# Kernel tuning notes

Hardware: AMD Instinct MI355X
Metric: run time of the kernel (lower is better)

The kernel has to match this reference:

```python
import jax, jax.numpy as jnp
import numpy as np

D_MODEL = 768
NUM_HEADS = 12
DIM_QKV = D_MODEL // NUM_HEADS  # 64
NEG_INF = -1000000000.0


def setup_inputs() -> dict:
    key = jax.random.key(0)
    ks = jax.random.split(key, 12)
    B, S = 2, 2048
    def lin(kw, kb):
        # torch nn.Linear default init: U(-1/sqrt(fan_in), 1/sqrt(fan_in))
        bound = 1.0 / np.sqrt(D_MODEL)
        W = jax.random.uniform(kw, (D_MODEL, D_MODEL), jnp.float32, -bound, bound)
        b = jax.random.uniform(kb, (D_MODEL,), jnp.float32, -bound, bound)
        return W, b
    Wq, bq = lin(ks[0], ks[1])
    Wk, bk = lin(ks[2], ks[3])
    Wv, bv = lin(ks[4], ks[5])
    Wo, bo = lin(ks[6], ks[7])
    Q = jax.random.normal(ks[8], (B, S, D_MODEL), jnp.float32)
    K = jax.random.normal(ks[9], (B, S, D_MODEL), jnp.float32)
    V = jax.random.normal(ks[10], (B, S, D_MODEL), jnp.float32)
    mask = jnp.tril(jnp.ones((S, S), dtype=bool))[None, None]  # [1,1,S,S] causal
    return {"Q": Q, "K": K, "V": V, "mask": mask,
            "Wq": Wq, "bq": bq, "Wk": Wk, "bk": bk,
            "Wv": Wv, "bv": bv, "Wo": Wo, "bo": bo}


def _split_heads(x):
    B, S, _ = x.shape
    return x.reshape(B, S, NUM_HEADS, DIM_QKV).transpose(0, 2, 1, 3)  # [B,H,S,d]


def reference(Q, K, V, mask, Wq, bq, Wk, bk, Wv, bv, Wo, bo):
    # torch Linear: y = x @ W.T + b
    q = _split_heads(Q @ Wq.T + bq)
    k = _split_heads(K @ Wk.T + bk)
    v = _split_heads(V @ Wv.T + bv)
    scale = jnp.sqrt(jnp.float32(DIM_QKV))
    scores = jnp.einsum('bhqd,bhkd->bhqk', q, k) / scale  # [B,H,S,S]
    scores = jnp.where(mask, scores, NEG_INF)
    probs = jax.nn.softmax(scores, axis=-1)  # dropout p=0 -> identity
    attn = jnp.einsum('bhqk,bhkd->bhqd', probs, v)
    B, H, S, d = attn.shape
    out = attn.transpose(0, 2, 1, 3).reshape(B, S, H * d) @ Wo.T + bo
    return out, scores
```

## Files before the change

### kernel.cpp

```cpp
#include <hip/hip_runtime.h>
#include <hip/hip_bf16.h>

typedef __attribute__((ext_vector_type(8))) short short8;
typedef __attribute__((ext_vector_type(4))) short short4v;
typedef __attribute__((ext_vector_type(4))) float f32x4;

#define S_LEN 2048
#define DM 768
#define NH 12
#define HD 64
#define NB 2
#define MROWS (NB*S_LEN)
#define NEGINF (-1.0e9f)
#define XEL 3145728
#define WEL 589824

__device__ __forceinline__ unsigned short f2bf(float x) {
    __hip_bfloat16 h = __float2bfloat16(x);
    return *reinterpret_cast<unsigned short*>(&h);
}

__device__ __forceinline__ void gl_lds16(const unsigned short* g, unsigned short* l) {
    __builtin_amdgcn_global_load_lds(
        (const __attribute__((address_space(1))) unsigned int*)g,
        (__attribute__((address_space(3))) unsigned int*)l, 16, 0, 0);
}

__global__ __launch_bounds__(256) void cvt_w_kernel(
    const float* w0, const float* w1, const float* w2, const float* w3,
    unsigned short* dst)
{
    int which = blockIdx.y;
    const float* src = (which == 0) ? w0 : (which == 1) ? w1 : (which == 2) ? w2 : w3;
    size_t idx = (size_t)blockIdx.x * 256 + threadIdx.x;
    const float* s = src + idx * 8;
    f32x4 v0 = *(const f32x4*)s;
    f32x4 v1 = *(const f32x4*)(s + 4);
    short8 o;
    o[0] = (short)f2bf(v0[0]); o[1] = (short)f2bf(v0[1]);
    o[2] = (short)f2bf(v0[2]); o[3] = (short)f2bf(v0[3]);
    o[4] = (short)f2bf(v1[0]); o[5] = (short)f2bf(v1[1]);
    o[6] = (short)f2bf(v1[2]); o[7] = (short)f2bf(v1[3]);
    *(short8*)&dst[(size_t)which * WEL + idx * 8] = o;
}

__global__ __launch_bounds__(256) void gemm_qkv_kernel(
    const float* Xq, const float* Xk, const float* Xv, const unsigned short* Wall,
    const float* b0, const float* b1, const float* b2, unsigned short* qh)
{
    int by = blockIdx.y;
    const float* A = (by == 0) ? Xq : (by == 1) ? Xk : Xv;
    const unsigned short* W = Wall + (size_t)by * WEL;
    const float* bias = (by == 0) ? b0 : (by == 1) ? b1 : b2;
    int bid = blockIdx.x;
    int im = bid & 31;
    int jn = bid >> 5;
    int i0 = im * 128, j0 = jn * 128;

    __shared__ unsigned short As[128 * 64];
    __shared__ unsigned short Ws[128 * 64];

    int t = threadIdx.x;
    int w = t >> 6, lane = t & 63, g = lane >> 4, fr = lane & 15;
    int wm = w >> 1, wn = w & 1;

    f32x4 acc[4][4];
    for (int i = 0; i < 4; ++i)
        for (int j = 0; j < 4; ++j)
            acc[i][j] = (f32x4){0.f, 0.f, 0.f, 0.f};

    int boff = t * 16;
    int arow = t >> 3;
    int acol = (t & 7) * 8;

    for (int k0 = 0; k0 < DM; k0 += 64) {
        __syncthreads();
        for (int r = 0; r < 4; ++r) {
            int b = r * 4096 + boff;
            int row = b >> 7, colb = b & 127;
            gl_lds16(&W[(size_t)(j0 + row) * DM + k0 + (colb >> 1)],
                     (unsigned short*)((char*)Ws + b));
        }
        for (int rr = 0; rr < 4; ++rr) {
            int row = rr * 32 + arow;
            const float* src = &A[(size_t)(i0 + row) * DM + k0 + acol];
            f32x4 v0 = *(const f32x4*)src;
            f32x4 v1 = *(const f32x4*)(src + 4);
            short8 o;
            o[0] = (short)f2bf(v0[0]); o[1] = (short)f2bf(v0[1]);
            o[2] = (short)f2bf(v0[2]); o[3] = (short)f2bf(v0[3]);
            o[4] = (short)f2bf(v1[0]); o[5] = (short)f2bf(v1[1]);
            o[6] = (short)f2bf(v1[2]); o[7] = (short)f2bf(v1[3]);
            *(short8*)&As[row * 64 + acol] = o;
        }
        __syncthreads();
        for (int kk = 0; kk < 2; ++kk) {
            short8 af[4], wf[4];
            for (int it = 0; it < 4; ++it)
                af[it] = *(const short8*)&As[(wm * 64 + it * 16 + fr) * 64 + kk * 32 + g * 8];
            for (int jt = 0; jt < 4; ++jt)
                wf[jt] = *(const short8*)&Ws[(wn * 64 + jt * 16 + fr) * 64 + kk * 32 + g * 8];
            for (int it = 0; it < 4; ++it)
                for (int jt = 0; jt < 4; ++jt)
                    acc[it][jt] = __builtin_amdgcn_mfma_f32_16x16x32_bf16(af[it], wf[jt], acc[it][jt], 0, 0, 0);
        }
    }

    float scl = (by == 0) ? 0.125f : 1.0f;
    if (by < 2) {
        unsigned short* outp = qh + (size_t)by * XEL;
        for (int jt = 0; jt < 4; ++jt) {
            int j = j0 + wn * 64 + jt * 16 + fr;
            float bv = bias[j];
            int h = j >> 6, dq = j & 63;
            for (int it = 0; it < 4; ++it)
                for (int r = 0; r < 4; ++r) {
                    int i = i0 + wm * 64 + it * 16 + g * 4 + r;
                    int bb = i >> 11, s = i & 2047;
                    outp[((size_t)((bb * NH + h) * S_LEN) + s) * HD + dq] = f2bf((acc[it][jt][r] + bv) * scl);
                }
        }
    } else {
        unsigned short* vtp = qh + (size_t)2 * XEL;
        for (int jt = 0; jt < 4; ++jt) {
            int j = j0 + wn * 64 + jt * 16 + fr;
            float bv = bias[j];
            int h = j >> 6, dq = j & 63;
            for (int it = 0; it < 4; ++it) {
                int ibase = i0 + wm * 64 + it * 16 + g * 4;
                int bb = ibase >> 11, s = ibase & 2047;
                short4v o;
                for (int r = 0; r < 4; ++r) o[r] = (short)f2bf(acc[it][jt][r] + bv);
                *(short4v*)&vtp[((size_t)(bb * NH + h) * HD + dq) * S_LEN + s] = o;
            }
        }
    }
}

__global__ __launch_bounds__(256) void gemm_o_kernel(
    const unsigned short* A, const unsigned short* W, const float* bias, float* f_out)
{
    int bid = blockIdx.x;
    int im = bid & 63;
    int jn = bid >> 6;
    int i0 = im * 64, j0 = jn * 64;

    __shared__ unsigned short As[64 * 64];
    __shared__ unsigned short Ws[64 * 64];

    int t = threadIdx.x;
    int w = t >> 6, lane = t & 63, g = lane >> 4, fr = lane & 15;
    int wm = w >> 1, wn = w & 1;

    f32x4 acc[2][2];
    for (int i = 0; i < 2; ++i)
        for (int j = 0; j < 2; ++j)
            acc[i][j] = (f32x4){0.f, 0.f, 0.f, 0.f};

    int boff = t * 16;

    for (int k0 = 0; k0 < DM; k0 += 64) {
        __syncthreads();
        for (int r = 0; r < 2; ++r) {
            int b = r * 4096 + boff;
            int row = b >> 7, colb = b & 127;
            gl_lds16(&A[(size_t)(i0 + row) * DM + k0 + (colb >> 1)],
                     (unsigned short*)((char*)As + b));
            gl_lds16(&W[(size_t)(j0 + row) * DM + k0 + (colb >> 1)],
                     (unsigned short*)((char*)Ws + b));
        }
        __syncthreads();
        for (int kk = 0; kk < 2; ++kk) {
            short8 af[2], wf[2];
            for (int it = 0; it < 2; ++it)
                af[it] = *(const short8*)&As[(wm * 32 + it * 16 + fr) * 64 + kk * 32 + g * 8];
            for (int jt = 0; jt < 2; ++jt)
                wf[jt] = *(const short8*)&Ws[(wn * 32 + jt * 16 + fr) * 64 + kk * 32 + g * 8];
            for (int it = 0; it < 2; ++it)
                for (int jt = 0; jt < 2; ++jt)
                    acc[it][jt] = __builtin_amdgcn_mfma_f32_16x16x32_bf16(af[it], wf[jt], acc[it][jt], 0, 0, 0);
        }
    }

    for (int jt = 0; jt < 2; ++jt) {
        int j = j0 + wn * 32 + jt * 16 + fr;
        float bv = bias[j];
        for (int it = 0; it < 2; ++it)
            for (int r = 0; r < 4; ++r) {
                int i = i0 + wm * 32 + it * 16 + g * 4 + r;
                f_out[(size_t)i * DM + j] = acc[it][jt][r] + bv;
            }
    }
}

__global__ __launch_bounds__(256) void attn_kernel(
    const unsigned short* q, const unsigned short* k, const unsigned short* vt,
    float* scores, unsigned short* attn)
{
    __shared__ unsigned short KV[2][8192];
    __shared__ float P[4][16][68];
    int t = threadIdx.x;
    int w = t >> 6, lane = t & 63, g = lane >> 4, fr = lane & 15;
    float (*Pw)[68] = P[w];

    int bid = blockIdx.x;
    int slot = bid >> 3;
    int bh = (bid & 7) * 3 + slot % 3;
    int j = 31 - slot / 3;
    int nt = j + 1;
    int qbase = j * 64 + w * 16;
    int b = bh / NH, h = bh % NH;

    const unsigned short* qp = q + (size_t)bh * S_LEN * HD;
    const unsigned short* kp = k + (size_t)bh * S_LEN * HD;
    const unsigned short* vp = vt + (size_t)bh * HD * S_LEN;
    float* sp = scores + (size_t)bh * S_LEN * S_LEN;

    int srow2 = t >> 3;
    int scb = (t & 7) * 16;

    short8 qf0 = *(const short8*)&qp[(size_t)(qbase + fr) * HD + g * 8];
    short8 qf1 = *(const short8*)&qp[(size_t)(qbase + fr) * HD + 32 + g * 8];

    f32x4 acc[4];
    for (int jt = 0; jt < 4; ++jt) acc[jt] = (f32x4){0.f, 0.f, 0.f, 0.f};
    float m_run = -1e30f, l_run = 0.f;

    int swzu = (fr & 7) * 8;

    {
        for (int rd = 0; rd < 2; ++rd) {
            int row = rd * 32 + srow2;
            int sc = (scb ^ ((row & 7) << 4)) >> 1;
            gl_lds16(&kp[(size_t)row * HD + sc], &KV[0][(size_t)t * 8 + rd * 2048]);
            gl_lds16(&vp[(size_t)row * S_LEN + sc], &KV[0][4096 + (size_t)t * 8 + rd * 2048]);
        }
    }

    int buf = 0;
    for (int kt = 0; kt < nt; ++kt) {
        __syncthreads();
        if (kt + 1 < nt) {
            int kb2 = (kt + 1) * 64;
            for (int rd = 0; rd < 2; ++rd) {
                int row = rd * 32 + srow2;
                int sc = (scb ^ ((row & 7) << 4)) >> 1;
                gl_lds16(&kp[(size_t)(kb2 + row) * HD + sc], &KV[buf ^ 1][(size_t)t * 8 + rd * 2048]);
                gl_lds16(&vp[(size_t)row * S_LEN + kb2 + sc], &KV[buf ^ 1][4096 + (size_t)t * 8 + rd * 2048]);
            }
        }
        const unsigned short* Kb = KV[buf];
        const unsigned short* Vb = KV[buf] + 4096;
        int kb = kt * 64;
        bool diag = (kt == nt - 1);

        short8 kf[4][2];
        for (int ktt = 0; ktt < 4; ++ktt) {
            int base = (ktt * 16 + fr) * 64;
            kf[ktt][0] = *(const short8*)&Kb[base + ((g * 8) ^ swzu)];
            kf[ktt][1] = *(const short8*)&Kb[base + ((32 + g * 8) ^ swzu)];
        }
        __builtin_amdgcn_s_setprio(1);
        f32x4 s4v[4];
        for (int ktt = 0; ktt < 4; ++ktt) {
            f32x4 s4 = (f32x4){0.f, 0.f, 0.f, 0.f};
            s4 = __builtin_amdgcn_mfma_f32_16x16x32_bf16(qf0, kf[ktt][0], s4, 0, 0, 0);
            s4 = __builtin_amdgcn_mfma_f32_16x16x32_bf16(qf1, kf[ktt][1], s4, 0, 0, 0);
            s4v[ktt] = s4;
        }
        __builtin_amdgcn_s_setprio(0);
        if (diag) {
            for (int ktt = 0; ktt < 4; ++ktt) {
                int kg = kb + ktt * 16 + fr;
                for (int r = 0; r < 4; ++r) {
                    int qg = qbase + g * 4 + r;
                    float val = (kg <= qg) ? s4v[ktt][r] : NEGINF;
                    Pw[g * 4 + r][ktt * 16 + fr] = val;
                }
            }
        } else {
            for (int ktt = 0; ktt < 4; ++ktt)
                for (int r = 0; r < 4; ++r)
                    Pw[g * 4 + r][ktt * 16 + fr] = s4v[ktt][r];
        }
        for (int pass = 0; pass < 4; ++pass) {
            int rr = pass * 4 + g;
            int cc = fr * 4;
            f32x4 vv = *(const f32x4*)&Pw[rr][cc];
            __builtin_nontemporal_store(vv, (f32x4*)&sp[(size_t)(qbase + rr) * S_LEN + kb + cc]);
        }
        f32x4 pA = *(const f32x4*)&Pw[fr][g * 8];
        f32x4 pB = *(const f32x4*)&Pw[fr][g * 8 + 4];
        f32x4 pC = *(const f32x4*)&Pw[fr][32 + g * 8];
        f32x4 pD = *(const f32x4*)&Pw[fr][32 + g * 8 + 4];
        float pv[16];
        pv[0]=pA[0]; pv[1]=pA[1]; pv[2]=pA[2]; pv[3]=pA[3];
        pv[4]=pB[0]; pv[5]=pB[1]; pv[6]=pB[2]; pv[7]=pB[3];
        pv[8]=pC[0]; pv[9]=pC[1]; pv[10]=pC[2]; pv[11]=pC[3];
        pv[12]=pD[0]; pv[13]=pD[1]; pv[14]=pD[2]; pv[15]=pD[3];
        float tmax = pv[0];
        for (int e = 1; e < 16; ++e) tmax = fmaxf(tmax, pv[e]);
        tmax = fmaxf(tmax, __shfl_xor(tmax, 16, 64));
        tmax = fmaxf(tmax, __shfl_xor(tmax, 32, 64));
        float m_new = fmaxf(m_run, tmax);
        float corr = __expf(m_run - m_new);
        float lsum = 0.f;
        for (int e = 0; e < 16; ++e) { pv[e] = __expf(pv[e] - m_new); lsum += pv[e]; }
        lsum += __shfl_xor(lsum, 16, 64);
        lsum += __shfl_xor(lsum, 32, 64);
        l_run = l_run * corr + lsum;
        m_run = m_new;
        short8 pa0, pa1;
        for (int e = 0; e < 8; ++e) { pa0[e] = (short)f2bf(pv[e]); pa1[e] = (short)f2bf(pv[8 + e]); }
        float fc[4];
        for (int r = 0; r < 4; ++r) fc[r] = __shfl(corr, g * 4 + r, 64);
        for (int jt = 0; jt < 4; ++jt)
            for (int r = 0; r < 4; ++r) acc[jt][r] *= fc[r];
        short8 vf[4][2];
        for (int jt = 0; jt < 4; ++jt) {
            int base = (jt * 16 + fr) * 64;
            vf[jt][0] = *(const short8*)&Vb[base + ((g * 8) ^ swzu)];
            vf[jt][1] = *(const short8*)&Vb[base + ((32 + g * 8) ^ swzu)];
        }
        __builtin_amdgcn_s_setprio(1);
        for (int jt = 0; jt < 4; ++jt) {
            acc[jt] = __builtin_amdgcn_mfma_f32_16x16x32_bf16(pa0, vf[jt][0], acc[jt], 0, 0, 0);
            acc[jt] = __builtin_amdgcn_mfma_f32_16x16x32_bf16(pa1, vf[jt][1], acc[jt], 0, 0, 0);
        }
        __builtin_amdgcn_s_setprio(0);
        buf ^= 1;
    }
    float linv[4];
    for (int r = 0; r < 4; ++r) linv[r] = 1.0f / __shfl(l_run, g * 4 + r, 64);
    for (int jt = 0; jt < 4; ++jt) {
        int col = h * HD + jt * 16 + fr;
        for (int r = 0; r < 4; ++r) {
            int i = b * S_LEN + qbase + g * 4 + r;
            attn[(size_t)i * DM + col] = f2bf(acc[jt][r] * linv[r]);
        }
    }
    f32x4 nv = (f32x4){NEGINF, NEGINF, NEGINF, NEGINF};
    int fill0 = nt * 64;
    for (int rr = 0; rr < 16; ++rr) {
        float* rowp = &sp[(size_t)(qbase + rr) * S_LEN];
        for (int c = fill0 + lane * 4; c < S_LEN; c += 256)
            __builtin_nontemporal_store(nv, (f32x4*)(rowp + c));
    }
}

extern "C" void kernel_launch(void* const* d_in, const int* in_sizes, int n_in,
                              void* d_out, int out_size, void* d_ws, size_t ws_size,
                              hipStream_t stream) {
    const float* Q  = (const float*)d_in[0];
    const float* K  = (const float*)d_in[1];
    const float* V  = (const float*)d_in[2];
    const float* Wq = (const float*)d_in[4];
    const float* bq = (const float*)d_in[5];
    const float* Wk = (const float*)d_in[6];
    const float* bk = (const float*)d_in[7];
    const float* Wv = (const float*)d_in[8];
    const float* bv = (const float*)d_in[9];
    const float* Wo = (const float*)d_in[10];
    const float* bo = (const float*)d_in[11];

    float* out = (float*)d_out;
    float* scores = out + (size_t)MROWS * DM;

    unsigned short* ws   = (unsigned short*)d_ws;
    unsigned short* Wbf  = ws;
    unsigned short* qh   = Wbf + (size_t)4 * WEL;
    unsigned short* attn = qh + (size_t)3 * XEL;

    cvt_w_kernel<<<dim3(288, 4), 256, 0, stream>>>(Wq, Wk, Wv, Wo, Wbf);
    gemm_qkv_kernel<<<dim3(192, 3), 256, 0, stream>>>(Q, K, V, Wbf, bq, bk, bv, qh);
    attn_kernel<<<dim3(768), 256, 0, stream>>>(qh, qh + (size_t)XEL, qh + (size_t)2 * XEL,
                                               scores, attn);
    gemm_o_kernel<<<dim3(768), 256, 0, stream>>>(attn, Wbf + (size_t)3 * WEL, bo, out);
}
```

Baseline: 168.3 us.

## Pair short and long causal query spans per attention block; swizzle GEMM tile order

Each attention block now has two waves take a 32-row query span from the short end of the causal triangle and two waves take one from the long end. This evens out work across blocks and removes the long-tail imbalance of per-diagonal scheduling. Waves whose span is finished skip compute but still join the shared K/V load loop and barriers, which idles some SIMDs inside the block and costs partial-tile masking work at 32-row granularity. The QKV and output GEMMs also remap block indices into 8-row groups so concurrently running blocks share A and W tiles in cache.

```diff
diff --git a/kernel.cpp b/kernel.cpp
--- a/kernel.cpp
+++ b/kernel.cpp
@@ -52,9 +52,9 @@
     const float* A = (by == 0) ? Xq : (by == 1) ? Xk : Xv;
     const unsigned short* W = Wall + (size_t)by * WEL;
     const float* bias = (by == 0) ? b0 : (by == 1) ? b1 : b2;
-    int bid = blockIdx.x;
-    int im = bid & 31;
-    int jn = bid >> 5;
+    int bx = blockIdx.x;
+    int im = (bx & 7) + 8 * (bx / 48);
+    int jn = (bx >> 3) % 6;
     int i0 = im * 128, j0 = jn * 128;
 
     __shared__ unsigned short As[128 * 64];
@@ -140,9 +140,9 @@
 __global__ __launch_bounds__(256) void gemm_o_kernel(
     const unsigned short* A, const unsigned short* W, const float* bias, float* f_out)
 {
-    int bid = blockIdx.x;
-    int im = bid & 63;
-    int jn = bid >> 6;
+    int bx = blockIdx.x;
+    int im = (bx & 7) + 8 * (bx / 96);
+    int jn = (bx >> 3) % 12;
     int i0 = im * 64, j0 = jn * 64;
 
     __shared__ unsigned short As[64 * 64];
@@ -204,11 +204,12 @@
     float (*Pw)[68] = P[w];
 
     int bid = blockIdx.x;
-    int slot = bid >> 3;
-    int bh = (bid & 7) * 3 + slot % 3;
-    int j = 31 - slot / 3;
-    int nt = j + 1;
-    int qbase = j * 64 + w * 16;
+    int bh = (bid & 7) * 3 + (bid >> 3) % 3;
+    int s = bid / 24;
+    int myspan = (w < 2) ? s : 63 - s;
+    int qbase = myspan * 32 + (w & 1) * 16;
+    int myNt = ((myspan * 32 + 31) >> 6) + 1;
+    int ntmax = (((63 - s) * 32 + 31) >> 6) + 1;
     int b = bh / NH, h = bh % NH;
 
     const unsigned short* qp = q + (size_t)bh * S_LEN * HD;
@@ -218,6 +219,7 @@
 
     int srow2 = t >> 3;
     int scb = (t & 7) * 16;
+    int swzu = (fr & 7) * 8;
 
     short8 qf0 = *(const short8*)&qp[(size_t)(qbase + fr) * HD + g * 8];
     short8 qf1 = *(const short8*)&qp[(size_t)(qbase + fr) * HD + 32 + g * 8];
@@ -226,21 +228,17 @@
     for (int jt = 0; jt < 4; ++jt) acc[jt] = (f32x4){0.f, 0.f, 0.f, 0.f};
     float m_run = -1e30f, l_run = 0.f;
 
-    int swzu = (fr & 7) * 8;
-
-    {
-        for (int rd = 0; rd < 2; ++rd) {
-            int row = rd * 32 + srow2;
-            int sc = (scb ^ ((row & 7) << 4)) >> 1;
-            gl_lds16(&kp[(size_t)row * HD + sc], &KV[0][(size_t)t * 8 + rd * 2048]);
-            gl_lds16(&vp[(size_t)row * S_LEN + sc], &KV[0][4096 + (size_t)t * 8 + rd * 2048]);
-        }
+    for (int rd = 0; rd < 2; ++rd) {
+        int row = rd * 32 + srow2;
+        int sc = (scb ^ ((row & 7) << 4)) >> 1;
+        gl_lds16(&kp[(size_t)row * HD + sc], &KV[0][(size_t)t * 8 + rd * 2048]);
+        gl_lds16(&vp[(size_t)row * S_LEN + sc], &KV[0][4096 + (size_t)t * 8 + rd * 2048]);
     }
 
     int buf = 0;
-    for (int kt = 0; kt < nt; ++kt) {
-        __syncthreads();
-        if (kt + 1 < nt) {
+    for (int kt = 0; kt < ntmax; ++kt) {
+        __syncthreads();
+        if (kt + 1 < ntmax) {
             int kb2 = (kt + 1) * 64;
             for (int rd = 0; rd < 2; ++rd) {
                 int row = rd * 32 + srow2;
@@ -249,85 +247,87 @@
                 gl_lds16(&vp[(size_t)row * S_LEN + kb2 + sc], &KV[buf ^ 1][4096 + (size_t)t * 8 + rd * 2048]);
             }
         }
-        const unsigned short* Kb = KV[buf];
-        const unsigned short* Vb = KV[buf] + 4096;
-        int kb = kt * 64;
-        bool diag = (kt == nt - 1);
-
-        short8 kf[4][2];
-        for (int ktt = 0; ktt < 4; ++ktt) {
-            int base = (ktt * 16 + fr) * 64;
-            kf[ktt][0] = *(const short8*)&Kb[base + ((g * 8) ^ swzu)];
-            kf[ktt][1] = *(const short8*)&Kb[base + ((32 + g * 8) ^ swzu)];
-        }
-        __builtin_amdgcn_s_setprio(1);
-        f32x4 s4v[4];
-        for (int ktt = 0; ktt < 4; ++ktt) {
-            f32x4 s4 = (f32x4){0.f, 0.f, 0.f, 0.f};
-            s4 = __builtin_amdgcn_mfma_f32_16x16x32_bf16(qf0, kf[ktt][0], s4, 0, 0, 0);
-            s4 = __builtin_amdgcn_mfma_f32_16x16x32_bf16(qf1, kf[ktt][1], s4, 0, 0, 0);
-            s4v[ktt] = s4;
-        }
-        __builtin_amdgcn_s_setprio(0);
-        if (diag) {
+        if (kt < myNt) {
+            const unsigned short* Kb = KV[buf];
+            const unsigned short* Vb = KV[buf] + 4096;
+            int kb = kt * 64;
+            bool diag = (kt == myNt - 1);
+
+            short8 kf[4][2];
             for (int ktt = 0; ktt < 4; ++ktt) {
-                int kg = kb + ktt * 16 + fr;
-                for (int r = 0; r < 4; ++r) {
-                    int qg = qbase + g * 4 + r;
-                    float val = (kg <= qg) ? s4v[ktt][r] : NEGINF;
-                    Pw[g * 4 + r][ktt * 16 + fr] = val;
+                int base = (ktt * 16 + fr) * 64;
+                kf[ktt][0] = *(const short8*)&Kb[base + ((g * 8) ^ swzu)];
+                kf[ktt][1] = *(const short8*)&Kb[base + ((32 + g * 8) ^ swzu)];
+            }
+            __builtin_amdgcn_s_setprio(1);
+            f32x4 s4v[4];
+            for (int ktt = 0; ktt < 4; ++ktt) {
+                f32x4 s4 = (f32x4){0.f, 0.f, 0.f, 0.f};
+                s4 = __builtin_amdgcn_mfma_f32_16x16x32_bf16(qf0, kf[ktt][0], s4, 0, 0, 0);
+                s4 = __builtin_amdgcn_mfma_f32_16x16x32_bf16(qf1, kf[ktt][1], s4, 0, 0, 0);
+                s4v[ktt] = s4;
+            }
+            __builtin_amdgcn_s_setprio(0);
+            if (diag) {
+                for (int ktt = 0; ktt < 4; ++ktt) {
+                    int kg = kb + ktt * 16 + fr;
+                    for (int r = 0; r < 4; ++r) {
+                        int qg = qbase + g * 4 + r;
+                        float val = (kg <= qg) ? s4v[ktt][r] : NEGINF;
+                        Pw[g * 4 + r][ktt * 16 + fr] = val;
+                    }
                 }
-            }
-        } else {
-            for (int ktt = 0; ktt < 4; ++ktt)
-                for (int r = 0; r < 4; ++r)
-                    Pw[g * 4 + r][ktt * 16 + fr] = s4v[ktt][r];
-        }
-        for (int pass = 0; pass < 4; ++pass) {
-            int rr = pass * 4 + g;
-            int cc = fr * 4;
-            f32x4 vv = *(const f32x4*)&Pw[rr][cc];
-            __builtin_nontemporal_store(vv, (f32x4*)&sp[(size_t)(qbase + rr) * S_LEN + kb + cc]);
-        }
-        f32x4 pA = *(const f32x4*)&Pw[fr][g * 8];
-        f32x4 pB = *(const f32x4*)&Pw[fr][g * 8 + 4];
-        f32x4 pC = *(const f32x4*)&Pw[fr][32 + g * 8];
-        f32x4 pD = *(const f32x4*)&Pw[fr][32 + g * 8 + 4];
-        float pv[16];
-        pv[0]=pA[0]; pv[1]=pA[1]; pv[2]=pA[2]; pv[3]=pA[3];
-        pv[4]=pB[0]; pv[5]=pB[1]; pv[6]=pB[2]; pv[7]=pB[3];
-        pv[8]=pC[0]; pv[9]=pC[1]; pv[10]=pC[2]; pv[11]=pC[3];
-        pv[12]=pD[0]; pv[13]=pD[1]; pv[14]=pD[2]; pv[15]=pD[3];
-        float tmax = pv[0];
-        for (int e = 1; e < 16; ++e) tmax = fmaxf(tmax, pv[e]);
-        tmax = fmaxf(tmax, __shfl_xor(tmax, 16, 64));
-        tmax = fmaxf(tmax, __shfl_xor(tmax, 32, 64));
-        float m_new = fmaxf(m_run, tmax);
-        float corr = __expf(m_run - m_new);
-        float lsum = 0.f;
-        for (int e = 0; e < 16; ++e) { pv[e] = __expf(pv[e] - m_new); lsum += pv[e]; }
-        lsum += __shfl_xor(lsum, 16, 64);
-        lsum += __shfl_xor(lsum, 32, 64);
-        l_run = l_run * corr + lsum;
-        m_run = m_new;
-        short8 pa0, pa1;
-        for (int e = 0; e < 8; ++e) { pa0[e] = (short)f2bf(pv[e]); pa1[e] = (short)f2bf(pv[8 + e]); }
-        float fc[4];
-        for (int r = 0; r < 4; ++r) fc[r] = __shfl(corr, g * 4 + r, 64);
-        for (int jt = 0; jt < 4; ++jt)
-            for (int r = 0; r < 4; ++r) acc[jt][r] *= fc[r];
-        short8 vf[4][2];
-        for (int jt = 0; jt < 4; ++jt) {
-            int base = (jt * 16 + fr) * 64;
-            vf[jt][0] = *(const short8*)&Vb[base + ((g * 8) ^ swzu)];
-            vf[jt][1] = *(const short8*)&Vb[base + ((32 + g * 8) ^ swzu)];
-        }
-        __builtin_amdgcn_s_setprio(1);
-        for (int jt = 0; jt < 4; ++jt) {
-            acc[jt] = __builtin_amdgcn_mfma_f32_16x16x32_bf16(pa0, vf[jt][0], acc[jt], 0, 0, 0);
-            acc[jt] = __builtin_amdgcn_mfma_f32_16x16x32_bf16(pa1, vf[jt][1], acc[jt], 0, 0, 0);
-        }
-        __builtin_amdgcn_s_setprio(0);
+            } else {
+                for (int ktt = 0; ktt < 4; ++ktt)
+                    for (int r = 0; r < 4; ++r)
+                        Pw[g * 4 + r][ktt * 16 + fr] = s4v[ktt][r];
+            }
+            for (int pass = 0; pass < 4; ++pass) {
+                int rr = pass * 4 + g;
+                int cc = fr * 4;
+                f32x4 vv = *(const f32x4*)&Pw[rr][cc];
+                __builtin_nontemporal_store(vv, (f32x4*)&sp[(size_t)(qbase + rr) * S_LEN + kb + cc]);
+            }
+            f32x4 pA = *(const f32x4*)&Pw[fr][g * 8];
+            f32x4 pB = *(const f32x4*)&Pw[fr][g * 8 + 4];
+            f32x4 pC = *(const f32x4*)&Pw[fr][32 + g * 8];
+            f32x4 pD = *(const f32x4*)&Pw[fr][32 + g * 8 + 4];
+            float pv[16];
+            pv[0]=pA[0]; pv[1]=pA[1]; pv[2]=pA[2]; pv[3]=pA[3];
+            pv[4]=pB[0]; pv[5]=pB[1]; pv[6]=pB[2]; pv[7]=pB[3];
+            pv[8]=pC[0]; pv[9]=pC[1]; pv[10]=pC[2]; pv[11]=pC[3];
+            pv[12]=pD[0]; pv[13]=pD[1]; pv[14]=pD[2]; pv[15]=pD[3];
+            float tmax = pv[0];
+            for (int e = 1; e < 16; ++e) tmax = fmaxf(tmax, pv[e]);
+            tmax = fmaxf(tmax, __shfl_xor(tmax, 16, 64));
+            tmax = fmaxf(tmax, __shfl_xor(tmax, 32, 64));
+            float m_new = fmaxf(m_run, tmax);
+            float corr = __expf(m_run - m_new);
+            float lsum = 0.f;
+            for (int e = 0; e < 16; ++e) { pv[e] = __expf(pv[e] - m_new); lsum += pv[e]; }
+            lsum += __shfl_xor(lsum, 16, 64);
+            lsum += __shfl_xor(lsum, 32, 64);
+            l_run = l_run * corr + lsum;
+            m_run = m_new;
+            short8 pa0, pa1;
+            for (int e = 0; e < 8; ++e) { pa0[e] = (short)f2bf(pv[e]); pa1[e] = (short)f2bf(pv[8 + e]); }
+            float fc[4];
+            for (int r = 0; r < 4; ++r) fc[r] = __shfl(corr, g * 4 + r, 64);
+            for (int jt = 0; jt < 4; ++jt)
+                for (int r = 0; r < 4; ++r) acc[jt][r] *= fc[r];
+            short8 vf[4][2];
+            for (int jt = 0; jt < 4; ++jt) {
+                int base = (jt * 16 + fr) * 64;
+                vf[jt][0] = *(const short8*)&Vb[base + ((g * 8) ^ swzu)];
+                vf[jt][1] = *(const short8*)&Vb[base + ((32 + g * 8) ^ swzu)];
+            }
+            __builtin_amdgcn_s_setprio(1);
+            for (int jt = 0; jt < 4; ++jt) {
+                acc[jt] = __builtin_amdgcn_mfma_f32_16x16x32_bf16(pa0, vf[jt][0], acc[jt], 0, 0, 0);
+                acc[jt] = __builtin_amdgcn_mfma_f32_16x16x32_bf16(pa1, vf[jt][1], acc[jt], 0, 0, 0);
+            }
+            __builtin_amdgcn_s_setprio(0);
+        }
         buf ^= 1;
     }
     float linv[4];
@@ -340,7 +340,7 @@
         }
     }
     f32x4 nv = (f32x4){NEGINF, NEGINF, NEGINF, NEGINF};
-    int fill0 = nt * 64;
+    int fill0 = myNt * 64;
     for (int rr = 0; rr < 16; ++rr) {
         float* rowp = &sp[(size_t)(qbase + rr) * S_LEN];
         for (int c = fill0 + lane * 4; c < S_LEN; c += 256)
```

Measured after the change: 157.5 us. -6.4%, faster.
